# Kernel tuning notes

Measured on AMD Instinct MI355X. Metric: run time of the kernel, lower is better.

Reference implementation:

```python
import jax, jax.numpy as jnp
import numpy as np

EPS = float(jnp.finfo(jnp.float32).eps)  # torch F.rms_norm default eps


def _rope(x, cos, sin):
    # x: [B,T,H,D]; cos/sin: [1,T,1,D//2]
    d = x.shape[-1] // 2
    x1, x2 = x[..., :d], x[..., d:]
    return jnp.concatenate([x1 * cos + x2 * sin, -x1 * sin + x2 * cos], axis=-1)


def _rmsnorm(x):
    ms = jnp.mean(jnp.square(x), axis=-1, keepdims=True)
    return x * jax.lax.rsqrt(ms + EPS)


def setup_inputs() -> dict:
    key = jax.random.key(0)
    ks = jax.random.split(key, 7)
    B, T, C, H, D = 2, 2048, 2048, 16, 128
    x = jax.random.normal(ks[0], (B, T, C), dtype=jnp.float32)
    # RoPE tables (use actual rotary angles for realism)
    pos = jnp.arange(T, dtype=jnp.float32)[:, None]
    inv_freq = 1.0 / (10000.0 ** (jnp.arange(0, D // 2, dtype=jnp.float32) / (D // 2)))
    ang = pos * inv_freq[None, :]  # [T, D/2]
    cos = jnp.cos(ang)[None, :, None, :]
    sin = jnp.sin(ang)[None, :, None, :]
    w_scale = 0.02
    wq = jax.random.normal(ks[1], (C, C), dtype=jnp.float32) * w_scale
    wk = jax.random.normal(ks[2], (C, C), dtype=jnp.float32) * w_scale
    wv = jax.random.normal(ks[3], (C, C), dtype=jnp.float32) * w_scale
    wproj = jax.random.normal(ks[4], (C, C), dtype=jnp.float32) * w_scale
    return {"x": x, "cos": cos, "sin": sin, "wq": wq, "wk": wk, "wv": wv, "wproj": wproj}


def reference(x, cos, sin, wq, wk, wv, wproj):
    B, T, C = x.shape
    H, D = 16, C // 16
    q = (x @ wq.T).reshape(B, T, H, D)
    k = (x @ wk.T).reshape(B, T, H, D)
    v = (x @ wv.T).reshape(B, T, H, D)
    q = _rmsnorm(_rope(q, cos, sin))
    k = _rmsnorm(_rope(k, cos, sin))
    scale = 1.0 / jnp.sqrt(jnp.asarray(D, dtype=x.dtype))
    # causal attention: logits [B,H,T,T]
    logits = jnp.einsum('bqhd,bkhd->bhqk', q, k) * scale
    causal = jnp.tril(jnp.ones((T, T), dtype=bool))
    logits = jnp.where(causal[None, None], logits, jnp.finfo(x.dtype).min)
    attn = jax.nn.softmax(logits, axis=-1)
    y = jnp.einsum('bhqk,bkhd->bqhd', attn, v).reshape(B, T, C)
    return y @ wproj.T
```

## Files before the change

kernel.cpp:

```cpp
#include <hip/hip_runtime.h>
#include <hip/hip_bf16.h>
#include <cstdint>
#include <cstddef>

typedef unsigned short u16;
typedef unsigned int u32;
typedef __attribute__((ext_vector_type(4))) float f32x4;
typedef __attribute__((ext_vector_type(8))) __bf16 bf16x8;

#define EPS_F 1.1920928955078125e-07f
#define INV_SQRT_D 0.08838834764831845f
#define LOG2E 1.4426950408889634f

__device__ __forceinline__ u16 f2bf(float f) {
  union { float f; u32 u; } v; v.f = f;
  u32 r = v.u + 0x7fffu + ((v.u >> 16) & 1u);
  return (u16)(r >> 16);
}

__device__ __forceinline__ ushort4 pack_bf4(float a, float b, float c, float d) {
  ushort4 o; o.x = f2bf(a); o.y = f2bf(b); o.z = f2bf(c); o.w = f2bf(d); return o;
}

__device__ __forceinline__ void gload_lds16(const void* g, void* l) {
  __builtin_amdgcn_global_load_lds((const __attribute__((address_space(1))) u32*)g,
                                   (__attribute__((address_space(3))) u32*)l, 16, 0, 0);
}

__global__ __launch_bounds__(256) void k_cast_bf16(const float* __restrict__ src,
                                                   u16* __restrict__ dst, int n) {
  int i = (blockIdx.x * 256 + threadIdx.x) * 4;
  if (i + 3 < n) {
    float4 v = *(const float4*)(src + i);
    *(ushort4*)(dst + i) = pack_bf4(v.x, v.y, v.z, v.w);
  }
}

__global__ __launch_bounds__(256) void k_gemm_bt(const u16* __restrict__ A,
                                                 const u16* __restrict__ Bw,
                                                 float* __restrict__ C,
                                                 int M, int N, int K) {
  __shared__ __align__(16) u16 As[128 * 32];
  __shared__ __align__(16) u16 Bs[128 * 32];
  const int tid = threadIdx.x;
  const int lane = tid & 63;
  const int wid = tid >> 6;
  const int wm = wid >> 1, wn = wid & 1;
  const int l15 = lane & 15, l4 = lane >> 4;

  f32x4 acc[4][4];
#pragma unroll
  for (int i = 0; i < 4; ++i)
#pragma unroll
    for (int j = 0; j < 4; ++j) acc[i][j] = {0.f, 0.f, 0.f, 0.f};

  const u16* Ab = A + (size_t)blockIdx.x * 128 * K;
  const u16* Bb = Bw + (size_t)blockIdx.y * 128 * K;
  const int lrow = lane >> 2;
  const int scol = ((lane & 3) ^ ((lane >> 3) & 3)) * 8;
  const int rswz = (l15 >> 1) & 3;

  for (int k0 = 0; k0 < K; k0 += 32) {
    __syncthreads();
#pragma unroll
    for (int p = 0; p < 2; ++p) {
      const int chunk = wid * 2 + p;
      const int row = chunk * 16 + lrow;
      gload_lds16(Ab + (size_t)row * K + k0 + scol, &As[chunk * 512]);
      gload_lds16(Bb + (size_t)row * K + k0 + scol, &Bs[chunk * 512]);
    }
    __syncthreads();
    bf16x8 af[4], bfv[4];
#pragma unroll
    for (int i = 0; i < 4; ++i) {
      const int cb = (l4 ^ rswz) * 8;
      af[i]  = *(const bf16x8*)&As[(wm * 64 + i * 16 + l15) * 32 + cb];
      bfv[i] = *(const bf16x8*)&Bs[(wn * 64 + i * 16 + l15) * 32 + cb];
    }
#pragma unroll
    for (int i = 0; i < 4; ++i)
#pragma unroll
      for (int j = 0; j < 4; ++j)
        acc[i][j] = __builtin_amdgcn_mfma_f32_16x16x32_bf16(af[i], bfv[j], acc[i][j], 0, 0, 0);
  }

  const int r0 = blockIdx.x * 128 + wm * 64 + l4 * 4;
  const int c0 = blockIdx.y * 128 + wn * 64 + l15;
#pragma unroll
  for (int i = 0; i < 4; ++i)
#pragma unroll
    for (int j = 0; j < 4; ++j) {
      float* Cp = C + (size_t)(r0 + i * 16) * N + c0 + j * 16;
#pragma unroll
      for (int r = 0; r < 4; ++r) Cp[(size_t)r * N] = acc[i][j][r];
    }
}

__global__ __launch_bounds__(256) void k_rope_rms(const float* __restrict__ qkv,
                                                  const float* __restrict__ cosp,
                                                  const float* __restrict__ sinp,
                                                  u16* __restrict__ qb, u16* __restrict__ kb,
                                                  u16* __restrict__ vb) {
  const int T = 2048;
  const int m = blockIdx.x;
  const int b = m >> 11;
  const int t = m & 2047;
  const int tid = threadIdx.x;
  const int h = tid >> 4;
  const int d0 = (tid & 15) * 4;
  const size_t ro = (size_t)m * 6144 + h * 128;

  float4 q1 = *(const float4*)(qkv + ro + d0);
  float4 q2 = *(const float4*)(qkv + ro + d0 + 64);
  float4 k1 = *(const float4*)(qkv + ro + 2048 + d0);
  float4 k2 = *(const float4*)(qkv + ro + 2048 + d0 + 64);
  float4 v1 = *(const float4*)(qkv + ro + 4096 + d0);
  float4 v2 = *(const float4*)(qkv + ro + 4096 + d0 + 64);
  float4 cs = *(const float4*)(cosp + (size_t)t * 64 + d0);
  float4 sn = *(const float4*)(sinp + (size_t)t * 64 + d0);

  float sq = q1.x*q1.x + q1.y*q1.y + q1.z*q1.z + q1.w*q1.w
           + q2.x*q2.x + q2.y*q2.y + q2.z*q2.z + q2.w*q2.w;
  float sk = k1.x*k1.x + k1.y*k1.y + k1.z*k1.z + k1.w*k1.w
           + k2.x*k2.x + k2.y*k2.y + k2.z*k2.z + k2.w*k2.w;
#pragma unroll
  for (int o = 1; o < 16; o <<= 1) {
    sq += __shfl_xor(sq, o, 64);
    sk += __shfl_xor(sk, o, 64);
  }
  const float rq = rsqrtf(sq * (1.f / 128.f) + EPS_F) * (INV_SQRT_D * LOG2E);
  const float rk = rsqrtf(sk * (1.f / 128.f) + EPS_F);

  const size_t ob = ((size_t)(b * 16 + h) * T + t) * 128 + d0;
  *(ushort4*)(qb + ob) = pack_bf4((q1.x*cs.x + q2.x*sn.x) * rq, (q1.y*cs.y + q2.y*sn.y) * rq,
                                  (q1.z*cs.z + q2.z*sn.z) * rq, (q1.w*cs.w + q2.w*sn.w) * rq);
  *(ushort4*)(qb + ob + 64) = pack_bf4((q2.x*cs.x - q1.x*sn.x) * rq, (q2.y*cs.y - q1.y*sn.y) * rq,
                                       (q2.z*cs.z - q1.z*sn.z) * rq, (q2.w*cs.w - q1.w*sn.w) * rq);
  *(ushort4*)(kb + ob) = pack_bf4((k1.x*cs.x + k2.x*sn.x) * rk, (k1.y*cs.y + k2.y*sn.y) * rk,
                                  (k1.z*cs.z + k2.z*sn.z) * rk, (k1.w*cs.w + k2.w*sn.w) * rk);
  *(ushort4*)(kb + ob + 64) = pack_bf4((k2.x*cs.x - k1.x*sn.x) * rk, (k2.y*cs.y - k1.y*sn.y) * rk,
                                       (k2.z*cs.z - k1.z*sn.z) * rk, (k2.w*cs.w - k1.w*sn.w) * rk);
  *(ushort4*)(vb + ob) = pack_bf4(v1.x, v1.y, v1.z, v1.w);
  *(ushort4*)(vb + ob + 64) = pack_bf4(v2.x, v2.y, v2.z, v2.w);
}

__global__ __launch_bounds__(256) void k_transpose_v(const u16* __restrict__ vb,
                                                     u16* __restrict__ vt) {
  const int T = 2048;
  __shared__ u16 tile[32][33];
  const int bh = blockIdx.z;
  const int t0 = blockIdx.x * 32;
  const int d0 = blockIdx.y * 32;
  const int tx = threadIdx.x & 31;
  const int ty = threadIdx.x >> 5;
  const size_t base = (size_t)bh * T * 128;
#pragma unroll
  for (int i = 0; i < 4; ++i)
    tile[ty + i * 8][tx] = vb[base + (size_t)(t0 + ty + i * 8) * 128 + d0 + tx];
  __syncthreads();
#pragma unroll
  for (int i = 0; i < 4; ++i)
    vt[base + (size_t)(d0 + ty + i * 8) * T + t0 + tx] = tile[tx][ty + i * 8];
}

__global__ __launch_bounds__(256) void k_attn(const u16* __restrict__ qb,
                                              const u16* __restrict__ kb,
                                              const u16* __restrict__ vt,
                                              u16* __restrict__ y) {
  const int T = 2048;
  __shared__ __align__(16) u16 Ks[2][64 * 128];
  __shared__ __align__(16) u16 Vs[2][128 * 64];
  __shared__ __align__(16) u16 Ps[64 * 72];

  const int tid = threadIdx.x;
  const int lane = tid & 63;
  const int wid = tid >> 6;
  const int bh = blockIdx.y;
  const int b = bh >> 4, h = bh & 15;
  const size_t hb = (size_t)bh * T * 128;
  const int l15 = lane & 15, l4 = lane >> 4;

  auto stage = [&](int it, int buf) {
#pragma unroll
    for (int p = 0; p < 4; ++p) {
      const int chunk = wid * 4 + p;
      {
        const int row = chunk * 4 + l4;
        const int scb = l15 ^ (row & 7);
        gload_lds16(kb + hb + (size_t)(it * 64 + row) * 128 + scb * 8, &Ks[buf][chunk * 512]);
      }
      {
        const int row = chunk * 8 + (lane >> 3);
        const int scb = (lane & 7) ^ (row & 7);
        gload_lds16(vt + hb + (size_t)row * T + it * 64 + scb * 8, &Vs[buf][chunk * 512]);
      }
    }
  };

#pragma unroll 1
  for (int ph = 0; ph < 2; ++ph) {
    const int qt = (ph == 0) ? (int)blockIdx.x : 31 - (int)blockIdx.x;
    const int q0 = qt * 64;
    const int niter = qt + 1;

    bf16x8 qf[4];
    {
      const int qrow = q0 + wid * 16 + l15;
#pragma unroll
      for (int ki = 0; ki < 4; ++ki)
        qf[ki] = *(const bf16x8*)(qb + hb + (size_t)qrow * 128 + ki * 32 + l4 * 8);
    }

    float mrow[4], lsum[4];
    f32x4 oacc[8];
#pragma unroll
    for (int r = 0; r < 4; ++r) { mrow[r] = -INFINITY; lsum[r] = 0.f; }
#pragma unroll
    for (int d = 0; d < 8; ++d) oacc[d] = {0.f, 0.f, 0.f, 0.f};

    stage(0, 0);
    asm volatile("s_waitcnt vmcnt(0)" ::: "memory");
    __builtin_amdgcn_s_barrier();
    __builtin_amdgcn_sched_barrier(0);

    int cur = 0;
#pragma unroll 1
    for (int it = 0; it < niter; ++it) {
      if (it + 1 < niter) stage(it + 1, cur ^ 1);

      f32x4 s[4];
#pragma unroll
      for (int ni = 0; ni < 4; ++ni) {
        s[ni] = {0.f, 0.f, 0.f, 0.f};
        const int r = ni * 16 + l15;
#pragma unroll
        for (int ki = 0; ki < 4; ++ki) {
          const int cb = (ki * 4 + l4) ^ (r & 7);
          bf16x8 kf = *(const bf16x8*)&Ks[cur][r * 128 + cb * 8];
          s[ni] = __builtin_amdgcn_mfma_f32_16x16x32_bf16(qf[ki], kf, s[ni], 0, 0, 0);
        }
      }

      if (it == niter - 1) {
        const int grow = q0 + wid * 16 + l4 * 4;
        const int gcol = it * 64 + l15;
#pragma unroll
        for (int ni = 0; ni < 4; ++ni)
#pragma unroll
          for (int r = 0; r < 4; ++r)
            if (gcol + ni * 16 > grow + r) s[ni][r] = -INFINITY;
      }

      float pv[4][4];
      float alpha[4];
#pragma unroll
      for (int r = 0; r < 4; ++r) {
        float mx = fmaxf(fmaxf(s[0][r], s[1][r]), fmaxf(s[2][r], s[3][r]));
#pragma unroll
        for (int o = 1; o < 16; o <<= 1) mx = fmaxf(mx, __shfl_xor(mx, o, 64));
        const float mnew = fmaxf(mrow[r], mx);
        alpha[r] = exp2f(mrow[r] - mnew);
        mrow[r] = mnew;
        float ps = 0.f;
#pragma unroll
        for (int ni = 0; ni < 4; ++ni) {
          const float p = exp2f(s[ni][r] - mnew);
          pv[ni][r] = p;
          ps += p;
        }
#pragma unroll
        for (int o = 1; o < 16; o <<= 1) ps += __shfl_xor(ps, o, 64);
        lsum[r] = lsum[r] * alpha[r] + ps;
      }
#pragma unroll
      for (int d = 0; d < 8; ++d) {
        f32x4 tv = oacc[d];
        tv[0] *= alpha[0]; tv[1] *= alpha[1]; tv[2] *= alpha[2]; tv[3] *= alpha[3];
        oacc[d] = tv;
      }
#pragma unroll
      for (int ni = 0; ni < 4; ++ni)
#pragma unroll
        for (int r = 0; r < 4; ++r)
          Ps[(wid * 16 + l4 * 4 + r) * 72 + ni * 16 + l15] = f2bf(pv[ni][r]);

#pragma unroll
      for (int k2 = 0; k2 < 2; ++k2) {
        bf16x8 pa = *(const bf16x8*)&Ps[(wid * 16 + l15) * 72 + k2 * 32 + l4 * 8];
#pragma unroll
        for (int dt = 0; dt < 8; ++dt) {
          const int r = dt * 16 + l15;
          const int cb = (k2 * 4 + l4) ^ (r & 7);
          bf16x8 vf = *(const bf16x8*)&Vs[cur][r * 64 + cb * 8];
          oacc[dt] = __builtin_amdgcn_mfma_f32_16x16x32_bf16(pa, vf, oacc[dt], 0, 0, 0);
        }
      }

      asm volatile("s_waitcnt vmcnt(0)" ::: "memory");
      __builtin_amdgcn_s_barrier();
      __builtin_amdgcn_sched_barrier(0);
      cur ^= 1;
    }

#pragma unroll
    for (int r = 0; r < 4; ++r) {
      const float inv = 1.f / lsum[r];
      const size_t yo = ((size_t)(b * T) + q0 + wid * 16 + l4 * 4 + r) * 2048 + h * 128;
#pragma unroll
      for (int dt = 0; dt < 8; ++dt)
        y[yo + dt * 16 + l15] = f2bf(oacc[dt][r] * inv);
    }
  }
}

extern "C" void kernel_launch(void* const* d_in, const int* in_sizes, int n_in,
                              void* d_out, int out_size, void* d_ws, size_t ws_size,
                              hipStream_t stream) {
  const float* x     = (const float*)d_in[0];
  const float* cosp  = (const float*)d_in[1];
  const float* sinp  = (const float*)d_in[2];
  const float* wq    = (const float*)d_in[3];
  const float* wk    = (const float*)d_in[4];
  const float* wv    = (const float*)d_in[5];
  const float* wproj = (const float*)d_in[6];
  float* out = (float*)d_out;

  const int T = 2048, C = 2048;
  const int M = 2 * T;
  const int N1 = 3 * C;

  char* ws = (char*)d_ws;
  size_t off = 0;
  auto take = [&](size_t bytes) -> char* {
    char* p = ws + off;
    off += (bytes + 255) & ~(size_t)255;
    return p;
  };
  u16* xb    = (u16*)take((size_t)M * C * 2);
  u16* wqkvb = (u16*)take((size_t)N1 * C * 2);
  u16* wpb   = (u16*)take((size_t)C * C * 2);
  float* qkv = (float*)take((size_t)M * N1 * 4);
  u16* qb    = (u16*)take((size_t)M * C * 2);
  u16* kb    = (u16*)take((size_t)M * C * 2);
  u16* vb    = (u16*)take((size_t)M * C * 2);
  u16* vt    = (u16*)take((size_t)M * C * 2);
  u16* yb    = (u16*)take((size_t)M * C * 2);
  (void)ws_size; (void)in_sizes; (void)n_in; (void)out_size;

  const int nx = M * C;
  const int nw = C * C;
  k_cast_bf16<<<nx / 1024, 256, 0, stream>>>(x, xb, nx);
  k_cast_bf16<<<nw / 1024, 256, 0, stream>>>(wq, wqkvb, nw);
  k_cast_bf16<<<nw / 1024, 256, 0, stream>>>(wk, wqkvb + (size_t)C * C, nw);
  k_cast_bf16<<<nw / 1024, 256, 0, stream>>>(wv, wqkvb + (size_t)2 * C * C, nw);
  k_cast_bf16<<<nw / 1024, 256, 0, stream>>>(wproj, wpb, nw);

  k_gemm_bt<<<dim3(M / 128, N1 / 128), 256, 0, stream>>>(xb, wqkvb, qkv, M, N1, C);
  k_rope_rms<<<M, 256, 0, stream>>>(qkv, cosp, sinp, qb, kb, vb);
  k_transpose_v<<<dim3(T / 32, 128 / 32, 32), 256, 0, stream>>>(vb, vt);
  k_attn<<<dim3(16, 32), 256, 0, stream>>>(qb, kb, vt, yb);
  k_gemm_bt<<<dim3(M / 128, C / 128), 256, 0, stream>>>(yb, wpb, out, M, C, C);
}
```

Baseline: 472.7 us.

## Use 256x256 pipelined bf16 GEMM for QKV projection with bf16 output

Adds a new 512-thread GEMM kernel with 256x256 tiles, double-buffered direct-to-LDS loads with XOR swizzle, and an interleaved barrier-scheduled MFMA pipeline, used for the fused QKV projection. The QKV intermediate is now stored as bf16 instead of fp32, halving the write and the rope/rmsnorm read traffic. This raises data reuse per tile and hides load latency, at the cost of fewer blocks (16x24 grid) and extra rounding of q/k/v before normalization.

```diff
diff --git a/kernel.cpp b/kernel.cpp
--- a/kernel.cpp
+++ b/kernel.cpp
@@ -17,15 +17,26 @@
   u32 r = v.u + 0x7fffu + ((v.u >> 16) & 1u);
   return (u16)(r >> 16);
 }
-
+__device__ __forceinline__ float bf2f(u16 u) {
+  union { u32 u; float f; } v; v.u = (u32)u << 16; return v.f;
+}
 __device__ __forceinline__ ushort4 pack_bf4(float a, float b, float c, float d) {
   ushort4 o; o.x = f2bf(a); o.y = f2bf(b); o.z = f2bf(c); o.w = f2bf(d); return o;
 }
-
+__device__ __forceinline__ float4 ld4bf(const u16* p) {
+  ushort4 u = *(const ushort4*)p;
+  float4 f; f.x = bf2f(u.x); f.y = bf2f(u.y); f.z = bf2f(u.z); f.w = bf2f(u.w); return f;
+}
 __device__ __forceinline__ void gload_lds16(const void* g, void* l) {
   __builtin_amdgcn_global_load_lds((const __attribute__((address_space(1))) u32*)g,
                                    (__attribute__((address_space(3))) u32*)l, 16, 0, 0);
 }
+
+#define MIDBAR() do { __builtin_amdgcn_s_barrier(); \
+  asm volatile("s_waitcnt lgkmcnt(0)" ::: "memory"); \
+  __builtin_amdgcn_sched_barrier(0); } while (0)
+#define ENDBAR() do { __builtin_amdgcn_s_barrier(); \
+  __builtin_amdgcn_sched_barrier(0); } while (0)
 
 __global__ __launch_bounds__(256) void k_cast_bf16(const float* __restrict__ src,
                                                    u16* __restrict__ dst, int n) {
@@ -34,6 +45,131 @@
     float4 v = *(const float4*)(src + i);
     *(ushort4*)(dst + i) = pack_bf4(v.x, v.y, v.z, v.w);
   }
+}
+
+__global__ __launch_bounds__(512, 2) void k_gemm256(const u16* __restrict__ A,
+                                                    const u16* __restrict__ Bw,
+                                                    u16* __restrict__ Cb,
+                                                    int M, int N, int K) {
+  __shared__ __align__(16) u16 As[2][2][8192];
+  __shared__ __align__(16) u16 Bs[2][2][8192];
+  const int tid = threadIdx.x;
+  const int lane = tid & 63;
+  const int wid = tid >> 6;
+  const int wm = wid >> 2;
+  const int wn = wid & 3;
+  const int l15 = lane & 15, l4 = lane >> 4;
+  const int nKt = K >> 6;
+  const int nIt = nKt >> 1;
+
+  const u16* Ab = A + (size_t)blockIdx.x * 256 * K;
+  const u16* Bb = Bw + (size_t)blockIdx.y * 256 * K;
+
+  f32x4 acc[8][4];
+#pragma unroll
+  for (int i = 0; i < 8; ++i)
+#pragma unroll
+    for (int j = 0; j < 4; ++j) acc[i][j] = {0.f, 0.f, 0.f, 0.f};
+
+  bf16x8 aReg[4][2];
+  bf16x8 bReg[2][2][2];
+
+  auto stage = [&](const u16* gbase, u16* slot) {
+#pragma unroll
+    for (int j = 0; j < 2; ++j) {
+      const int idx = j * 512 + tid;
+      const int row = idx >> 3;
+      const int gg = (idx & 7) ^ (row & 7);
+      gload_lds16(gbase + (size_t)row * K + gg * 8,
+                  slot + (size_t)(j * 512 + wid * 64) * 8);
+    }
+  };
+  auto ldA = [&](int buf, int mh) {
+    const u16* base = As[buf][wm];
+#pragma unroll
+    for (int mf = 0; mf < 4; ++mf) {
+      const int rh = (mh * 4 + mf) * 16 + l15;
+#pragma unroll
+      for (int kk = 0; kk < 2; ++kk) {
+        const int g = (kk * 4 + l4) ^ (rh & 7);
+        aReg[mf][kk] = *(const bf16x8*)&base[rh * 64 + g * 8];
+      }
+    }
+  };
+  auto ldB = [&](int buf, int nh) {
+    const u16* base = Bs[buf][wn >> 1];
+#pragma unroll
+    for (int nf = 0; nf < 2; ++nf) {
+      const int rh = (wn & 1) * 64 + (nh * 2 + nf) * 16 + l15;
+#pragma unroll
+      for (int kk = 0; kk < 2; ++kk) {
+        const int g = (kk * 4 + l4) ^ (rh & 7);
+        bReg[nh][nf][kk] = *(const bf16x8*)&base[rh * 64 + g * 8];
+      }
+    }
+  };
+  auto mm = [&](int mh, int nh) {
+    __builtin_amdgcn_s_setprio(1);
+#pragma unroll
+    for (int kk = 0; kk < 2; ++kk)
+#pragma unroll
+      for (int mf = 0; mf < 4; ++mf)
+#pragma unroll
+        for (int nf = 0; nf < 2; ++nf)
+          acc[mh * 4 + mf][nh * 2 + nf] = __builtin_amdgcn_mfma_f32_16x16x32_bf16(
+              aReg[mf][kk], bReg[nh][nf][kk], acc[mh * 4 + mf][nh * 2 + nf], 0, 0, 0);
+    __builtin_amdgcn_s_setprio(0);
+  };
+
+  const size_t hK = (size_t)128 * K;
+  stage(Bb, &Bs[0][0][0]);
+  stage(Bb + hK, &Bs[0][1][0]);
+  stage(Ab, &As[0][0][0]);
+  stage(Ab + hK, &As[0][1][0]);
+  stage(Bb + 64, &Bs[1][0][0]);
+  stage(Bb + hK + 64, &Bs[1][1][0]);
+  asm volatile("s_waitcnt vmcnt(4)" ::: "memory");
+  __builtin_amdgcn_s_barrier();
+  __builtin_amdgcn_sched_barrier(0);
+
+#pragma unroll 1
+  for (int i = 0; i < nIt; ++i) {
+    const int t1 = 2 * i + 1;
+    const int t2 = (2 * i + 2 < nKt) ? 2 * i + 2 : nKt - 1;
+    const int t3 = (2 * i + 3 < nKt) ? 2 * i + 3 : nKt - 1;
+    const size_t o1 = (size_t)t1 * 64, o2 = (size_t)t2 * 64, o3 = (size_t)t3 * 64;
+
+    ldA(0, 0); ldB(0, 0); stage(Ab + o1, &As[1][0][0]);
+    MIDBAR(); mm(0, 0); ENDBAR();
+    ldB(0, 1); stage(Ab + hK + o1, &As[1][1][0]);
+    MIDBAR(); mm(0, 1); ENDBAR();
+    ldA(0, 1); stage(Bb + o2, &Bs[0][0][0]);
+    MIDBAR(); mm(1, 1); ENDBAR();
+    stage(Bb + hK + o2, &Bs[0][1][0]);
+    MIDBAR(); mm(1, 0);
+    asm volatile("s_waitcnt vmcnt(4)" ::: "memory");
+    ENDBAR();
+    ldA(1, 0); ldB(1, 0); stage(Ab + o2, &As[0][0][0]);
+    MIDBAR(); mm(0, 0); ENDBAR();
+    ldB(1, 1); stage(Ab + hK + o2, &As[0][1][0]);
+    MIDBAR(); mm(0, 1); ENDBAR();
+    ldA(1, 1); stage(Bb + o3, &Bs[1][0][0]);
+    MIDBAR(); mm(1, 1); ENDBAR();
+    stage(Bb + hK + o3, &Bs[1][1][0]);
+    MIDBAR(); mm(1, 0);
+    asm volatile("s_waitcnt vmcnt(4)" ::: "memory");
+    ENDBAR();
+  }
+
+  const int r0 = blockIdx.x * 256 + wm * 128 + l4 * 4;
+  const int c0 = blockIdx.y * 256 + wn * 64 + l15;
+#pragma unroll
+  for (int i2 = 0; i2 < 8; ++i2)
+#pragma unroll
+    for (int j2 = 0; j2 < 4; ++j2)
+#pragma unroll
+      for (int r = 0; r < 4; ++r)
+        Cb[(size_t)(r0 + i2 * 16 + r) * N + c0 + j2 * 16] = f2bf(acc[i2][j2][r]);
 }
 
 __global__ __launch_bounds__(256) void k_gemm_bt(const u16* __restrict__ A,
@@ -96,7 +232,7 @@
     }
 }
 
-__global__ __launch_bounds__(256) void k_rope_rms(const float* __restrict__ qkv,
+__global__ __launch_bounds__(256) void k_rope_rms(const u16* __restrict__ qkv,
                                                   const float* __restrict__ cosp,
                                                   const float* __restrict__ sinp,
                                                   u16* __restrict__ qb, u16* __restrict__ kb,
@@ -110,12 +246,12 @@
   const int d0 = (tid & 15) * 4;
   const size_t ro = (size_t)m * 6144 + h * 128;
 
-  float4 q1 = *(const float4*)(qkv + ro + d0);
-  float4 q2 = *(const float4*)(qkv + ro + d0 + 64);
-  float4 k1 = *(const float4*)(qkv + ro + 2048 + d0);
-  float4 k2 = *(const float4*)(qkv + ro + 2048 + d0 + 64);
-  float4 v1 = *(const float4*)(qkv + ro + 4096 + d0);
-  float4 v2 = *(const float4*)(qkv + ro + 4096 + d0 + 64);
+  float4 q1 = ld4bf(qkv + ro + d0);
+  float4 q2 = ld4bf(qkv + ro + d0 + 64);
+  float4 k1 = ld4bf(qkv + ro + 2048 + d0);
+  float4 k2 = ld4bf(qkv + ro + 2048 + d0 + 64);
+  float4 v1 = ld4bf(qkv + ro + 4096 + d0);
+  float4 v2 = ld4bf(qkv + ro + 4096 + d0 + 64);
   float4 cs = *(const float4*)(cosp + (size_t)t * 64 + d0);
   float4 sn = *(const float4*)(sinp + (size_t)t * 64 + d0);
 
@@ -339,7 +475,7 @@
   u16* xb    = (u16*)take((size_t)M * C * 2);
   u16* wqkvb = (u16*)take((size_t)N1 * C * 2);
   u16* wpb   = (u16*)take((size_t)C * C * 2);
-  float* qkv = (float*)take((size_t)M * N1 * 4);
+  u16* qkvb  = (u16*)take((size_t)M * N1 * 2);
   u16* qb    = (u16*)take((size_t)M * C * 2);
   u16* kb    = (u16*)take((size_t)M * C * 2);
   u16* vb    = (u16*)take((size_t)M * C * 2);
@@ -355,8 +491,8 @@
   k_cast_bf16<<<nw / 1024, 256, 0, stream>>>(wv, wqkvb + (size_t)2 * C * C, nw);
   k_cast_bf16<<<nw / 1024, 256, 0, stream>>>(wproj, wpb, nw);
 
-  k_gemm_bt<<<dim3(M / 128, N1 / 128), 256, 0, stream>>>(xb, wqkvb, qkv, M, N1, C);
-  k_rope_rms<<<M, 256, 0, stream>>>(qkv, cosp, sinp, qb, kb, vb);
+  k_gemm256<<<dim3(M / 256, N1 / 256), 512, 0, stream>>>(xb, wqkvb, qkvb, M, N1, C);
+  k_rope_rms<<<M, 256, 0, stream>>>(qkvb, cosp, sinp, qb, kb, vb);
   k_transpose_v<<<dim3(T / 32, 128 / 32, 32), 256, 0, stream>>>(vb, vt);
   k_attn<<<dim3(16, 32), 256, 0, stream>>>(qb, kb, vt, yb);
   k_gemm_bt<<<dim3(M / 128, C / 128), 256, 0, stream>>>(yb, wpb, out, M, C, C);
```

Result: faster. 447.8 us (-5.3%).
